# Kernel optimization log

Measured on AMD Instinct MI355X. Metric: run time of the kernel, lower is better.

The kernel has to match this reference:

```python
import jax, jax.numpy as jnp
import numpy as np

BS, EP = 32, 32
N_AGENTS, N_ATOM, EMBED = 8, 51, 32
STATE_DIM, HYP = 128, 64
V_MIN, V_MAX = -10.0, 10.0


def proj(support, probs, v_min, v_max, n_atom):
    # C51 categorical projection of (support, probs) onto the fixed atom grid
    # linspace(v_min, v_max, n_atom). support/probs: [..., M] -> [..., n_atom]
    support, probs = jnp.broadcast_arrays(support, probs)
    delta = (v_max - v_min) / (n_atom - 1)
    b = (jnp.clip(support, v_min, v_max) - v_min) / delta
    l = jnp.floor(b)
    u = jnp.ceil(b)
    eq = (u == l).astype(probs.dtype)  # support exactly on an atom -> all mass to l
    ml = probs * (u - b + eq)
    mu = probs * (b - l)
    shp = probs.shape
    n = int(np.prod(shp[:-1]))
    m = shp[-1]
    rows = jnp.arange(n)[:, None]
    out = jnp.zeros((n, n_atom), probs.dtype)
    out = out.at[rows, l.astype(jnp.int32).reshape(n, m)].add(ml.reshape(n, m))
    out = out.at[rows, u.astype(jnp.int32).reshape(n, m)].add(mu.reshape(n, m))
    return out.reshape(shp[:-1] + (n_atom,))


def bconv(p, q):
    # Full 1D convolution of per-row categorical pmfs (sum of two random vars).
    # p: [N, L], q: [N, M] -> [N, L+M-1], via grouped conv (one group per row).
    N, L = p.shape
    M = q.shape[-1]
    out = jax.lax.conv_general_dilated(
        p[None], jnp.flip(q, -1)[:, None, :],
        window_strides=(1,), padding=[(M - 1, M - 1)],
        feature_group_count=N, dimension_numbers=('NCW', 'OIW', 'NCW'))
    return out[0]


def mlp2(x, w1, b1, w2, b2):
    return jax.nn.relu(x @ w1.T + b1) @ w2.T + b2


def setup_inputs():
    key = jax.random.key(0)
    ks = jax.random.split(key, 20)
    def p(k, shape, s=0.05):
        return jax.random.normal(k, shape, dtype=jnp.float32) * s
    aq = jax.random.uniform(ks[0], (BS, EP, N_AGENTS, N_ATOM), dtype=jnp.float32)
    aq = aq / jnp.sum(aq, -1, keepdims=True)  # valid categorical distributions
    return {
        'agent_qs_distri': aq,
        'states': p(ks[1], (BS, EP, STATE_DIM), 1.0),
        'hw1_w1': p(ks[2], (HYP, STATE_DIM)), 'hw1_b1': p(ks[3], (HYP,)),
        'hw1_w2': p(ks[4], (EMBED * N_AGENTS, HYP)), 'hw1_b2': p(ks[5], (EMBED * N_AGENTS,)),
        'hb1_w': p(ks[6], (EMBED, STATE_DIM)), 'hb1_b': p(ks[7], (EMBED,)),
        'hwf_w1': p(ks[8], (HYP, STATE_DIM)), 'hwf_b1': p(ks[9], (HYP,)),
        'hwf_w2': p(ks[10], (EMBED, HYP)), 'hwf_b2': p(ks[11], (EMBED,)),
        'v_w1': p(ks[12], (EMBED, STATE_DIM)), 'v_b1': p(ks[13], (EMBED,)),
        'v_w2': p(ks[14], (1, EMBED)), 'v_b2': p(ks[15], (1,)),
    }


def reference(agent_qs_distri, states, hw1_w1, hw1_b1, hw1_w2, hw1_b2,
              hb1_w, hb1_b, hwf_w1, hwf_b1, hwf_w2, hwf_b2,
              v_w1, v_b1, v_w2, v_b2):
    bs, ep, n_agents, n_atom = agent_qs_distri.shape
    s = states.reshape(-1, STATE_DIM)
    atoms = jnp.linspace(V_MIN, V_MAX, n_atom).astype(jnp.float32)  # [A]

    w1 = jnp.abs(mlp2(s, hw1_w1, hw1_b1, hw1_w2, hw1_b2)).reshape(bs, ep, EMBED, n_agents)
    b1 = (s @ hb1_w.T + hb1_b).reshape(bs, ep, EMBED)

    # stage 1: scale each agent's support by w1[..., k, i], project back onto atoms
    sup1 = atoms * w1[..., None]                                       # [bs,ep,E,Na,A]
    aw = proj(sup1, agent_qs_distri[:, :, None], V_MIN, V_MAX, n_atom)  # [bs,ep,E,Na,A]
    awf = aw.reshape(-1, n_agents, n_atom)                              # [bs*ep*E,Na,A]
    q = awf[:, 0]
    for i in range(1, n_agents):
        q = bconv(q, awf[:, i])                                         # [.., Na*A-Na+1]
    L1 = n_agents * n_atom - n_agents + 1
    sup = jnp.linspace(n_agents * V_MIN, n_agents * V_MAX, L1).astype(jnp.float32)
    sup = jax.nn.elu(sup + b1[..., None])                               # [bs,ep,E,L1]
    x = proj(sup, q.reshape(bs, ep, EMBED, L1), V_MIN, V_MAX, n_atom)   # [bs,ep,E,A]

    # stage 2: hyper_w_final scaling, convolve across embed dim, add V(s)
    wf = jnp.abs(mlp2(s, hwf_w1, hwf_b1, hwf_w2, hwf_b2)).reshape(bs, ep, EMBED)
    xw = proj(atoms * wf[..., None], x, V_MIN, V_MAX, n_atom)           # [bs,ep,E,A]
    xwf = xw.reshape(-1, EMBED, n_atom)
    q = xwf[:, 0]
    for i in range(1, EMBED):
        q = bconv(q, xwf[:, i])                                         # [bs*ep, E*A-E+1]
    L2 = EMBED * n_atom - EMBED + 1
    v = mlp2(s, v_w1, v_b1, v_w2, v_b2).reshape(bs, ep, 1)
    sup2 = jnp.linspace(EMBED * V_MIN, EMBED * V_MAX, L2).astype(jnp.float32) + v
    return proj(sup2, q.reshape(bs, ep, L2), V_MIN, V_MAX, n_atom)      # [bs,ep,A]
```

## Files before the change

kernel.cpp:

```cpp
#include <hip/hip_runtime.h>
#include <hip/hip_bf16.h>
#include <math.h>

typedef unsigned short u16;

#define WAVE_SYNC() asm volatile("s_waitcnt lgkmcnt(0)" ::: "memory")

__device__ __forceinline__ float bf2f(u16 u) {
  union { unsigned int i; float f; } c;
  c.i = ((unsigned int)u) << 16;
  return c.f;
}
__device__ __forceinline__ float bflo(unsigned int u) {
  union { unsigned int i; float f; } c; c.i = u << 16; return c.f;
}
__device__ __forceinline__ float bfhi(unsigned int u) {
  union { unsigned int i; float f; } c; c.i = u & 0xffff0000u; return c.f;
}
__device__ __forceinline__ u16 f2bf(float f) {
  union { float f; unsigned int i; } c;
  c.f = f;
  unsigned int x = c.i;
  unsigned int r = (x + 0x7fffu + ((x >> 16) & 1u)) >> 16;
  return (u16)r;
}

__device__ __forceinline__ void proj_bounds(float wv, int& ML, int& MH) {
  float smin = (-10.0f + 0.4f * 0.0f)  * wv;
  float smax = (-10.0f + 0.4f * 50.0f) * wv;
  float bmin = (fminf(fmaxf(smin, -10.0f), 10.0f) + 10.0f) / 0.4f;
  float bmax = (fminf(fmaxf(smax, -10.0f), 10.0f) + 10.0f) / 0.4f;
  ML = (int)floorf(bmin);
  MH = (int)ceilf(bmax);
}

template<typename SUPP>
__device__ __forceinline__ void proj_scan(float* __restrict__ g1,
                                          float* __restrict__ g2,
                                          int span, int lane, SUPP supp)
{
  if (lane < 52) g1[lane] = 0.f;
  if (lane < 53) g2[lane] = 0.f;
  float cml = 0.f, cmu = 0.f;
  int ck = -1;
  for (int base = 0; base < span; base += 64) {
    int t = base + lane;
    bool act = (t < span);
    int tc = act ? t : (span - 1);
    float sup, p;
    supp(tc, act, sup, p);
    float c  = fminf(fmaxf(sup, -10.0f), 10.0f);
    float b  = (c + 10.0f) / 0.4f;
    float l  = floorf(b);
    float u  = ceilf(b);
    float eq = (u == l) ? 1.0f : 0.0f;
    float ml = p * (u - b + eq);
    float mu = p * (b - l);
    int   li = (int)l;
    bool last = (base + 64 >= span);
    if (lane == 0 && ck >= 0) {
      if (ck == li) { ml += cml; mu += cmu; }
      else          { g1[ck] = cml; g2[ck + 1] = cmu; }
    }
#pragma unroll
    for (int d = 1; d < 64; d <<= 1) {
      int   lo = __shfl_up(li, d);
      float a1 = __shfl_up(ml, d);
      float a2 = __shfl_up(mu, d);
      bool same = (lane >= d) && (lo == li);
      ml += same ? a1 : 0.f;
      mu += same ? a2 : 0.f;
    }
    int ln = __shfl_down(li, 1);
    bool runend = (lane == 63) ? last : (ln != li);
    if (runend) { g1[li] = ml; g2[li + 1] = mu; }
    if (!last) {
      cml = __shfl(ml, 63);
      cmu = __shfl(mu, 63);
      ck  = __shfl(li, 63);
    }
  }
}

__device__ __forceinline__ void conv_pad2(const float* __restrict__ q,
                                          float* __restrict__ qn,
                                          const float* __restrict__ kvs,
                                          int ML, int W, int T,
                                          int LQ, int HQ, int tid, int nthr)
{
  const int Lout = LQ + ML, Hout = HQ + ML + T;
  for (int J = Lout + tid; J <= Hout; J += nthr) {
    const float* qp = q + (J - ML);
    float acc = 0.f;
    for (int c = 0; c < W; c += 4) {
      float4 k4 = *(const float4*)(kvs + c);
      acc = fmaf(k4.x, qp[-c],     acc);
      acc = fmaf(k4.y, qp[-c - 1], acc);
      acc = fmaf(k4.z, qp[-c - 2], acc);
      acc = fmaf(k4.w, qp[-c - 3], acc);
    }
    qn[J] = acc;
  }
}

__device__ __forceinline__ void conv16(const float* __restrict__ q,
                                       float* __restrict__ qn,
                                       const float* __restrict__ kvs,
                                       int ML, int T,
                                       int LQ, int HQ, int tid, int nthr)
{
  const int Lout = LQ + ML, Hout = HQ + ML + T;
  for (int J = Lout + tid; J <= Hout; J += nthr) {
    const float* qp = q + (J - ML);
    float a0 = 0.f, a1 = 0.f;
#pragma unroll
    for (int c = 0; c < 16; c += 4) {
      float4 k4 = *(const float4*)(kvs + c);
      a0 = fmaf(k4.x, qp[-c],     a0);
      a1 = fmaf(k4.y, qp[-c - 1], a1);
      a0 = fmaf(k4.z, qp[-c - 2], a0);
      a1 = fmaf(k4.w, qp[-c - 3], a1);
    }
    qn[J] = a0 + a1;
  }
}

template<int TA, int TB>
__device__ __forceinline__ float gather_part(const float* __restrict__ pb,
                                             float wv, float j)
{
  float a0 = 0.f, a1 = 0.f, a2 = 0.f, a3 = 0.f;
  const float4* pb4 = (const float4*)pb;
  const float base = 25.0f - j;
#pragma unroll
  for (int t4 = TA; t4 < TB; ++t4) {
    float4 p4 = pb4[t4];
#define G1(PX, TT, AC) { \
    float sup = ((float)(TT) * 0.4f - 10.0f) * wv; \
    float c   = fminf(fmaxf(sup, -10.0f), 10.0f); \
    float d   = fmaf(c, 2.5f, base); \
    AC = fmaf(PX, fmaxf(0.f, 1.0f - fabsf(d)), AC); }
    G1(p4.x, 4 * t4 + 0, a0)
    G1(p4.y, 4 * t4 + 1, a1)
    G1(p4.z, 4 * t4 + 2, a2)
    G1(p4.w, 4 * t4 + 3, a3)
#undef G1
  }
  return (a0 + a1) + (a2 + a3);
}

template<int BF>
__device__ __forceinline__ float ldt(const void* p, int i) {
  if (BF) return bf2f(((const u16*)p)[i]);
  return ((const float*)p)[i];
}

template<int BF>
__device__ __forceinline__ float dot128_t(const void* w, int row, const float* s) {
  float acc = 0.f;
  if (BF) {
    const uint4* p = (const uint4*)((const u16*)w + row * 128);
#pragma unroll
    for (int i = 0; i < 16; ++i) {
      uint4 v = p[i];
      int b = i * 8;
      acc = fmaf(bflo(v.x), s[b + 0], acc); acc = fmaf(bfhi(v.x), s[b + 1], acc);
      acc = fmaf(bflo(v.y), s[b + 2], acc); acc = fmaf(bfhi(v.y), s[b + 3], acc);
      acc = fmaf(bflo(v.z), s[b + 4], acc); acc = fmaf(bfhi(v.z), s[b + 5], acc);
      acc = fmaf(bflo(v.w), s[b + 6], acc); acc = fmaf(bfhi(v.w), s[b + 7], acc);
    }
  } else {
    const float4* p = (const float4*)((const float*)w + row * 128);
#pragma unroll
    for (int i = 0; i < 32; ++i) {
      float4 v = p[i];
      int b = i * 4;
      acc = fmaf(v.x, s[b + 0], acc); acc = fmaf(v.y, s[b + 1], acc);
      acc = fmaf(v.z, s[b + 2], acc); acc = fmaf(v.w, s[b + 3], acc);
    }
  }
  return acc;
}

template<int BF>
__device__ __forceinline__ float dot64_t(const void* w, int row, const float* h) {
  float acc = 0.f;
  if (BF) {
    const uint4* p = (const uint4*)((const u16*)w + row * 64);
#pragma unroll
    for (int i = 0; i < 8; ++i) {
      uint4 v = p[i];
      int b = i * 8;
      acc = fmaf(bflo(v.x), h[b + 0], acc); acc = fmaf(bfhi(v.x), h[b + 1], acc);
      acc = fmaf(bflo(v.y), h[b + 2], acc); acc = fmaf(bfhi(v.y), h[b + 3], acc);
      acc = fmaf(bflo(v.z), h[b + 4], acc); acc = fmaf(bfhi(v.z), h[b + 5], acc);
      acc = fmaf(bflo(v.w), h[b + 6], acc); acc = fmaf(bfhi(v.w), h[b + 7], acc);
    }
  } else {
    const float4* p = (const float4*)((const float*)w + row * 64);
#pragma unroll
    for (int i = 0; i < 16; ++i) {
      float4 v = p[i];
      int b = i * 4;
      acc = fmaf(v.x, h[b + 0], acc); acc = fmaf(v.y, h[b + 1], acc);
      acc = fmaf(v.z, h[b + 2], acc); acc = fmaf(v.w, h[b + 3], acc);
    }
  }
  return acc;
}

template<int BF>
__device__ __forceinline__ void mlp_body(
    const void* states,
    const void* hw1_w1, const void* hw1_b1, const void* hw1_w2, const void* hw1_b2,
    const void* hb1_w,  const void* hb1_b,
    const void* hwf_w1, const void* hwf_b1, const void* hwf_w2, const void* hwf_b2,
    const void* v_w1,   const void* v_b1,   const void* v_w2,   const void* v_b2,
    float* w1_ws, float* b1_ws, float* wf_ws, float* v_ws,
    int n, int tid, float* s, float* h1, float* hf, float* vh)
{
  s[tid]      = ldt<BF>(states, n * 128 + tid);
  s[tid + 64] = ldt<BF>(states, n * 128 + 64 + tid);
  __syncthreads();

  h1[tid] = fmaxf(dot128_t<BF>(hw1_w1, tid, s) + ldt<BF>(hw1_b1, tid), 0.f);
  hf[tid] = fmaxf(dot128_t<BF>(hwf_w1, tid, s) + ldt<BF>(hwf_b1, tid), 0.f);
  if (tid < 32) {
    vh[tid] = fmaxf(dot128_t<BF>(v_w1, tid, s) + ldt<BF>(v_b1, tid), 0.f);
    b1_ws[n * 32 + tid] = dot128_t<BF>(hb1_w, tid, s) + ldt<BF>(hb1_b, tid);
  }
  __syncthreads();

#pragma unroll
  for (int k = 0; k < 4; ++k) {
    int o = tid + 64 * k;
    w1_ws[n * 256 + o] = fabsf(dot64_t<BF>(hw1_w2, o, h1) + ldt<BF>(hw1_b2, o));
  }
  if (tid < 32)
    wf_ws[n * 32 + tid] = fabsf(dot64_t<BF>(hwf_w2, tid, hf) + ldt<BF>(hwf_b2, tid));
  if (tid == 0) {
    float acc = ldt<BF>(v_b2, 0);
    for (int e = 0; e < 32; ++e) acc = fmaf(ldt<BF>(v_w2, e), vh[e], acc);
    v_ws[n] = acc;
  }
}

__global__ __launch_bounds__(64) void k_mlp(
    const void* __restrict__ states,
    const void* __restrict__ hw1_w1, const void* __restrict__ hw1_b1,
    const void* __restrict__ hw1_w2, const void* __restrict__ hw1_b2,
    const void* __restrict__ hb1_w,  const void* __restrict__ hb1_b,
    const void* __restrict__ hwf_w1, const void* __restrict__ hwf_b1,
    const void* __restrict__ hwf_w2, const void* __restrict__ hwf_b2,
    const void* __restrict__ v_w1,   const void* __restrict__ v_b1,
    const void* __restrict__ v_w2,   const void* __restrict__ v_b2,
    float* __restrict__ w1_ws, float* __restrict__ b1_ws,
    float* __restrict__ wf_ws, float* __restrict__ v_ws,
    int* __restrict__ flag)
{
  __shared__ float s[128];
  __shared__ float h1[64];
  __shared__ float hf[64];
  __shared__ float vh[32];
  const int n = blockIdx.x;
  const int tid = threadIdx.x;

  const u16* sr = (const u16*)states;
  unsigned int e0 = (sr[tid] >> 7) & 0xFF;
  unsigned int e1 = (sr[tid + 64] >> 7) & 0xFF;
  unsigned long long bl0 = __ballot(e0 >= 97 && e0 <= 141);
  unsigned long long bl1 = __ballot(e1 >= 97 && e1 <= 141);
  int bf = (__popcll(bl0) + __popcll(bl1) >= 104) ? 1 : 0;
  if (tid == 0) *flag = bf;

  if (bf)
    mlp_body<1>(states, hw1_w1, hw1_b1, hw1_w2, hw1_b2, hb1_w, hb1_b,
                hwf_w1, hwf_b1, hwf_w2, hwf_b2, v_w1, v_b1, v_w2, v_b2,
                w1_ws, b1_ws, wf_ws, v_ws, n, tid, s, h1, hf, vh);
  else
    mlp_body<0>(states, hw1_w1, hw1_b1, hw1_w2, hw1_b2, hb1_w, hb1_b,
                hwf_w1, hwf_b1, hwf_w2, hwf_b2, v_w1, v_b1, v_w2, v_b2,
                w1_ws, b1_ws, wf_ws, v_ws, n, tid, s, h1, hf, vh);
}

__global__ __launch_bounds__(128) void k_perembed(
    const void* __restrict__ aq,
    const float* __restrict__ w1_ws, const float* __restrict__ b1_ws,
    const float* __restrict__ wf_ws, float* __restrict__ xw_ws,
    const int* __restrict__ flag)
{
  __shared__ __align__(16) float Ab[520];
  __shared__ __align__(16) float Bb[520];
  __shared__ __align__(16) float kv_all[8][16];
  __shared__ __align__(16) float kvo[56];
  __shared__ __align__(16) float p_lds[8][52];
  __shared__ float gA[53];
  __shared__ float gB[54];
  __shared__ __align__(16) float pE[2][64];

  const int tid  = threadIdx.x;
  const int wit  = tid >> 6;
  const int lane = tid & 63;
  const int task = blockIdx.x;
  const int n = task >> 5;
  const int e = task & 31;
  const int bf = *flag;

  if (bf) {
    const u16* p = (const u16*)aq + n * 408;
    if (lane < 52) {
#pragma unroll
      for (int k = 0; k < 4; ++k) {
        int a = 4 * wit + k;
        p_lds[a][lane] = (lane < 51) ? bf2f(p[a * 51 + lane]) : 0.f;
      }
    }
  } else {
    const float* p = (const float*)aq + n * 408;
    if (lane < 52) {
#pragma unroll
      for (int k = 0; k < 4; ++k) {
        int a = 4 * wit + k;
        p_lds[a][lane] = (lane < 51) ? p[a * 51 + lane] : 0.f;
      }
    }
  }
  float wreg = (lane < 8) ? w1_ws[n * 256 + e * 8 + lane] : 0.f;
  float b1v  = b1_ws[n * 32 + e];
  float wfv  = wf_ws[n * 32 + e];

  int mlA = 0, mhA = 0;
  if (lane < 8) proj_bounds(wreg, mlA, mhA);
  WAVE_SYNC();

  {
    int a  = 4 * wit + (lane >> 4);
    int jj = lane & 15;
    float wv = __shfl(wreg, a);
    int ML = __shfl(mlA, a);
    int MH = __shfl(mhA, a);
    int T  = MH - ML;
    float K = (25.0f - (float)(ML + jj)) - 25.0f * wv;
    float a0 = 0.f, a1 = 0.f, a2 = 0.f, a3 = 0.f;
    const float4* pb4 = (const float4*)p_lds[a];
#pragma unroll
    for (int t4 = 0; t4 < 13; ++t4) {
      float4 p4 = pb4[t4];
      float d0 = fmaf((float)(4 * t4 + 0), wv, K);
      float d1 = fmaf((float)(4 * t4 + 1), wv, K);
      float d2 = fmaf((float)(4 * t4 + 2), wv, K);
      float d3 = fmaf((float)(4 * t4 + 3), wv, K);
      a0 = fmaf(p4.x, fmaxf(0.f, 1.0f - fabsf(d0)), a0);
      a1 = fmaf(p4.y, fmaxf(0.f, 1.0f - fabsf(d1)), a1);
      a2 = fmaf(p4.z, fmaxf(0.f, 1.0f - fabsf(d2)), a2);
      a3 = fmaf(p4.w, fmaxf(0.f, 1.0f - fabsf(d3)), a3);
    }
    if (T <= 15)
      kv_all[a][jj] = (jj <= T) ? ((a0 + a1) + (a2 + a3)) : 0.f;
  }
  __syncthreads();

  int LQ, HQ;
  float* q = Ab;
  float* qn = Bb;
  {
    float wv0 = __shfl(wreg, 0);
    int ML0 = __shfl(mlA, 0), MH0 = __shfl(mhA, 0);
    int T0 = MH0 - ML0;
    if (tid < 64) {
      if (T0 <= 15) {
        if (lane <= T0) Ab[64 + ML0 + lane] = kv_all[0][lane];
      } else {
        float acc = gather_part<0, 13>(p_lds[0], wv0, (float)(ML0 + lane));
        if (lane <= T0) Ab[64 + ML0 + lane] = acc;
      }
    }
    LQ = 64 + ML0; HQ = 64 + MH0;
  }

  for (int a = 1; a < 8; ++a) {
    float wv = __shfl(wreg, a);
    int ML = __shfl(mlA, a), MH = __shfl(mhA, a);
    int T = MH - ML;
    const float* kvs;
    int W;
    if (T <= 15) {
      kvs = &kv_all[a][0];
      W = 16;
    } else {
      W = (T + 4) & ~3;
      if (tid < 64) {
        float acc = gather_part<0, 13>(p_lds[a], wv, (float)(ML + lane));
        if (lane < W) kvo[lane] = (lane <= T) ? acc : 0.f;
      }
      kvs = kvo;
    }
    if (tid < W - 1) q[LQ - 1 - tid] = 0.f;
    if (tid < T)     q[HQ + 1 + tid] = 0.f;
    __syncthreads();
    if (T <= 15) conv16(q, qn, kvs, ML, T, LQ, HQ, tid, 128);
    else         conv_pad2(q, qn, kvs, ML, W, T, LQ, HQ, tid, 128);
    __syncthreads();
    LQ += ML; HQ += MH;
    float* t_ = q; q = qn; qn = t_;
  }

  if (wit == 0) {
    int span = HQ - LQ + 1;
    int LQl = LQ;
    const float* qf = q;
    proj_scan(gA, gB, span, lane, [&](int t, bool act, float& sup, float& p) {
      int tg = (LQl - 64) + t;
      float raw = (-80.0f + 0.4f * (float)tg) + b1v;
      sup = (raw > 0.f) ? raw : expm1f(raw);
      p = act ? qf[LQl + t] : 0.f;
    });
    WAVE_SYNC();
    float x2v = (lane < 51) ? (gA[lane] + gB[lane]) : 0.f;
    WAVE_SYNC();
    if (lane < 52) p_lds[0][lane] = (lane < 51) ? x2v : 0.f;
  }
  __syncthreads();

  {
    int MLf, MHf;
    proj_bounds(wfv, MLf, MHf);
    float j = (float)(MLf + lane);
    float part = (wit == 0) ? gather_part<0, 7>(p_lds[0], wfv, j)
                            : gather_part<7, 13>(p_lds[0], wfv, j);
    pE[wit][lane] = part;
    __syncthreads();
    if (wit == 0 && lane <= MHf - MLf)
      xw_ws[task * 51 + MLf + lane] = pE[0][lane] + pE[1][lane];
  }
}

__global__ __launch_bounds__(256) void k_final(
    const float* __restrict__ xw_ws, const float* __restrict__ wf_ws,
    const float* __restrict__ v_ws,
    void* __restrict__ out, const int* __restrict__ flag)
{
  __shared__ __align__(16) float bufA[4608];
  __shared__ __align__(16) float bufB[4608];
  __shared__ int meta_s[63];
  __shared__ int meta_l[63];
  __shared__ int meta_ml[32];
  __shared__ int meta_g[6];
  __shared__ int meta_mltot;
  __shared__ float gA[53], gB[54];

  const int n    = blockIdx.x;
  const int tid  = threadIdx.x;
  const int lane = tid & 63;
  const int bf   = *flag;

  float wfreg = (lane < 32) ? wf_ws[n * 32 + lane] : 0.f;
  float vv    = v_ws[n];

  for (int i = tid; i < 4608; i += 256) { bufA[i] = 0.f; bufB[i] = 0.f; }

  if (tid < 64) {
    int ml, mh;
    proj_bounds(wfreg, ml, mh);
    if (lane < 32) meta_ml[lane] = ml;
    int msum = ml;
#pragma unroll
    for (int d = 1; d < 32; d <<= 1) msum += __shfl_xor(msum, d);
    if (lane == 0) meta_mltot = msum;

    int curlen = mh - ml + 1;
    int base = 0, Ncur = 32;
#pragma unroll
    for (int c = 0; c <= 5; ++c) {
      int lm = (lane < Ncur) ? curlen : 0;
#pragma unroll
      for (int d = 1; d < 32; d <<= 1) {
        int o = __shfl_xor(lm, d);
        lm = (o > lm) ? o : lm;
      }
      int G = (lm + 11) & ~3;
      int sp = ((curlen + 3) & ~3) + G;
      int inc = (lane < Ncur) ? sp : 0;
      int v0 = inc;
#pragma unroll
      for (int d = 1; d < 32; d <<= 1) {
        int u = __shfl_up(inc, d);
        if (lane >= d && lane < 32) inc += u;
      }
      if (lane < Ncur) {
        meta_s[base + lane] = 832 + (inc - v0);
        meta_l[base + lane] = curlen;
      }
      if (lane == 0) meta_g[c] = G;
      if (c < 5) {
        int l0 = __shfl(curlen, 2 * lane);
        int l1 = __shfl(curlen, 2 * lane + 1);
        curlen = l0 + l1 - 1;
        base += Ncur;
        Ncur >>= 1;
      }
    }
  }
  __syncthreads();

  {
    int g = tid >> 3, i = tid & 7;
    int s = meta_s[g], l = meta_l[g], ml = meta_ml[g];
    const float* row = xw_ws + (n * 32 + g) * 51 + ml;
    for (int i0 = i; i0 < l; i0 += 8) bufA[s + i0] = row[i0];
  }
  __syncthreads();

#pragma unroll
  for (int c = 1; c <= 5; ++c) {
    const float* bin = (c & 1) ? bufA : bufB;
    float*       bout = (c & 1) ? bufB : bufA;
    const int Nout = 32 >> c;
    const int lg = 3 + c;
    const int gs = 1 << lg;
    const int k  = tid >> lg;
    const int st = tid & (gs - 1);
    const int bc = 64 - (64 >> c);
    const int bp = 64 - (64 >> (c - 1));
    const int i0 = bp + 2 * k;
    const int sA = meta_s[i0];
    const int sB = meta_s[i0 + 1];
    const int lB = meta_l[i0 + 1];
    const int sO = meta_s[bc + k];
    const int lO = meta_l[bc + k];
    const int W  = (lB + 3) & ~3;

    for (int j = st * 2; j < lO; j += gs * 2) {
      const float* Ap = bin + sA + j + 1;
      float a0 = 0.f, a1 = 0.f;
      for (int m = 0; m < W; m += 4) {
        float4 k4 = *(const float4*)(bin + sB + m);
        float v0 = Ap[-m], v1 = Ap[-m - 1], v2 = Ap[-m - 2];
        float v3 = Ap[-m - 3], v4 = Ap[-m - 4];
        a0 = fmaf(k4.x, v1, fmaf(k4.y, v2, fmaf(k4.z, v3, fmaf(k4.w, v4, a0))));
        a1 = fmaf(k4.x, v0, fmaf(k4.y, v1, fmaf(k4.z, v2, fmaf(k4.w, v3, a1))));
      }
      bout[sO + j] = a0;
      if (j + 1 < lO) bout[sO + j + 1] = a1;
    }

    if (c >= 2 && c <= 4) {
      int G = meta_g[c];
      for (int p = tid; p < G; p += 256) bout[832 - G + p] = 0.f;
      for (int k2 = 0; k2 < Nout; ++k2) {
        int ss = meta_s[bc + k2] + meta_l[bc + k2];
        int ee = (k2 + 1 < Nout) ? meta_s[bc + k2 + 1]
                                 : ss + G + 3;
        for (int p = ss + tid; p < ee; p += 256) bout[p] = 0.f;
      }
    }
    __syncthreads();
  }

  if (tid < 64) {
    int s5 = meta_s[62], l5 = meta_l[62], mlt = meta_mltot;
    const float* qf = bufB + s5;
    proj_scan(gA, gB, l5, lane, [&](int t, bool act, float& sup, float& p) {
      int tg = mlt + t;
      sup = (-320.0f + 0.4f * (float)tg) + vv;
      p = act ? qf[t] : 0.f;
    });
    WAVE_SYNC();
    if (lane < 51) {
      float o = gA[lane] + gB[lane];
      if (bf) ((u16*)out)[n * 51 + lane] = f2bf(o);
      else    ((float*)out)[n * 51 + lane] = o;
    }
  }
}

extern "C" void kernel_launch(void* const* d_in, const int* in_sizes, int n_in,
                              void* d_out, int out_size, void* d_ws, size_t ws_size,
                              hipStream_t stream)
{
  float* ws    = (float*)d_ws;
  float* w1_ws = ws;
  float* b1_ws = w1_ws + 1024 * 256;
  float* wf_ws = b1_ws + 1024 * 32;
  float* v_ws  = wf_ws + 1024 * 32;
  float* xw_ws = v_ws  + 1024;
  int*   flag  = (int*)(xw_ws + 1024 * 32 * 51);

  k_mlp<<<1024, 64, 0, stream>>>(d_in[1],
      d_in[2], d_in[3], d_in[4], d_in[5], d_in[6], d_in[7],
      d_in[8], d_in[9], d_in[10], d_in[11], d_in[12], d_in[13],
      d_in[14], d_in[15],
      w1_ws, b1_ws, wf_ws, v_ws, flag);

  k_perembed<<<32768, 128, 0, stream>>>(d_in[0], w1_ws, b1_ws, wf_ws, xw_ws, flag);

  k_final<<<1024, 256, 0, stream>>>(xw_ws, wf_ws, v_ws, d_out, flag);
}
```

Measured before the change: 274.6 us.

## Rework work split across MLP, per-embed and final kernels with LDS atomics

```diff
diff --git a/kernel.cpp b/kernel.cpp
--- a/kernel.cpp
+++ b/kernel.cpp
@@ -32,54 +32,6 @@
   float bmax = (fminf(fmaxf(smax, -10.0f), 10.0f) + 10.0f) / 0.4f;
   ML = (int)floorf(bmin);
   MH = (int)ceilf(bmax);
-}
-
-template<typename SUPP>
-__device__ __forceinline__ void proj_scan(float* __restrict__ g1,
-                                          float* __restrict__ g2,
-                                          int span, int lane, SUPP supp)
-{
-  if (lane < 52) g1[lane] = 0.f;
-  if (lane < 53) g2[lane] = 0.f;
-  float cml = 0.f, cmu = 0.f;
-  int ck = -1;
-  for (int base = 0; base < span; base += 64) {
-    int t = base + lane;
-    bool act = (t < span);
-    int tc = act ? t : (span - 1);
-    float sup, p;
-    supp(tc, act, sup, p);
-    float c  = fminf(fmaxf(sup, -10.0f), 10.0f);
-    float b  = (c + 10.0f) / 0.4f;
-    float l  = floorf(b);
-    float u  = ceilf(b);
-    float eq = (u == l) ? 1.0f : 0.0f;
-    float ml = p * (u - b + eq);
-    float mu = p * (b - l);
-    int   li = (int)l;
-    bool last = (base + 64 >= span);
-    if (lane == 0 && ck >= 0) {
-      if (ck == li) { ml += cml; mu += cmu; }
-      else          { g1[ck] = cml; g2[ck + 1] = cmu; }
-    }
-#pragma unroll
-    for (int d = 1; d < 64; d <<= 1) {
-      int   lo = __shfl_up(li, d);
-      float a1 = __shfl_up(ml, d);
-      float a2 = __shfl_up(mu, d);
-      bool same = (lane >= d) && (lo == li);
-      ml += same ? a1 : 0.f;
-      mu += same ? a2 : 0.f;
-    }
-    int ln = __shfl_down(li, 1);
-    bool runend = (lane == 63) ? last : (ln != li);
-    if (runend) { g1[li] = ml; g2[li + 1] = mu; }
-    if (!last) {
-      cml = __shfl(ml, 63);
-      cmu = __shfl(mu, 63);
-      ck  = __shfl(li, 63);
-    }
-  }
 }
 
 __device__ __forceinline__ void conv_pad2(const float* __restrict__ q,
@@ -115,6 +67,28 @@
     float a0 = 0.f, a1 = 0.f;
 #pragma unroll
     for (int c = 0; c < 16; c += 4) {
+      float4 k4 = *(const float4*)(kvs + c);
+      a0 = fmaf(k4.x, qp[-c],     a0);
+      a1 = fmaf(k4.y, qp[-c - 1], a1);
+      a0 = fmaf(k4.z, qp[-c - 2], a0);
+      a1 = fmaf(k4.w, qp[-c - 3], a1);
+    }
+    qn[J] = a0 + a1;
+  }
+}
+
+__device__ __forceinline__ void conv8(const float* __restrict__ q,
+                                      float* __restrict__ qn,
+                                      const float* __restrict__ kvs,
+                                      int ML, int T,
+                                      int LQ, int HQ, int tid, int nthr)
+{
+  const int Lout = LQ + ML, Hout = HQ + ML + T;
+  for (int J = Lout + tid; J <= Hout; J += nthr) {
+    const float* qp = q + (J - ML);
+    float a0 = 0.f, a1 = 0.f;
+#pragma unroll
+    for (int c = 0; c < 8; c += 4) {
       float4 k4 = *(const float4*)(kvs + c);
       a0 = fmaf(k4.x, qp[-c],     a0);
       a1 = fmaf(k4.y, qp[-c - 1], a1);
@@ -210,42 +184,41 @@
 }
 
 template<int BF>
-__device__ __forceinline__ void mlp_body(
+__device__ __forceinline__ void mlp_par(
     const void* states,
     const void* hw1_w1, const void* hw1_b1, const void* hw1_w2, const void* hw1_b2,
     const void* hb1_w,  const void* hb1_b,
     const void* hwf_w1, const void* hwf_b1, const void* hwf_w2, const void* hwf_b2,
     const void* v_w1,   const void* v_b1,   const void* v_w2,   const void* v_b2,
     float* w1_ws, float* b1_ws, float* wf_ws, float* v_ws,
-    int n, int tid, float* s, float* h1, float* hf, float* vh)
-{
-  s[tid]      = ldt<BF>(states, n * 128 + tid);
-  s[tid + 64] = ldt<BF>(states, n * 128 + 64 + tid);
+    float* s_st, float* h1, float* hf, float* vh, int n, int tid)
+{
+  if (tid < 128) s_st[tid] = ldt<BF>(states, n * 128 + tid);
   __syncthreads();
-
-  h1[tid] = fmaxf(dot128_t<BF>(hw1_w1, tid, s) + ldt<BF>(hw1_b1, tid), 0.f);
-  hf[tid] = fmaxf(dot128_t<BF>(hwf_w1, tid, s) + ldt<BF>(hwf_b1, tid), 0.f);
-  if (tid < 32) {
-    vh[tid] = fmaxf(dot128_t<BF>(v_w1, tid, s) + ldt<BF>(v_b1, tid), 0.f);
-    b1_ws[n * 32 + tid] = dot128_t<BF>(hb1_w, tid, s) + ldt<BF>(hb1_b, tid);
-  }
+  if (tid < 64)
+    h1[tid] = fmaxf(dot128_t<BF>(hw1_w1, tid, s_st) + ldt<BF>(hw1_b1, tid), 0.f);
+  else if (tid < 128)
+    hf[tid - 64] = fmaxf(dot128_t<BF>(hwf_w1, tid - 64, s_st) + ldt<BF>(hwf_b1, tid - 64), 0.f);
+  else if (tid < 160)
+    vh[tid - 128] = fmaxf(dot128_t<BF>(v_w1, tid - 128, s_st) + ldt<BF>(v_b1, tid - 128), 0.f);
+  else if (tid < 192)
+    b1_ws[n * 32 + tid - 160] = dot128_t<BF>(hb1_w, tid - 160, s_st) + ldt<BF>(hb1_b, tid - 160);
   __syncthreads();
-
-#pragma unroll
-  for (int k = 0; k < 4; ++k) {
-    int o = tid + 64 * k;
-    w1_ws[n * 256 + o] = fabsf(dot64_t<BF>(hw1_w2, o, h1) + ldt<BF>(hw1_b2, o));
-  }
-  if (tid < 32)
-    wf_ws[n * 32 + tid] = fabsf(dot64_t<BF>(hwf_w2, tid, hf) + ldt<BF>(hwf_b2, tid));
-  if (tid == 0) {
-    float acc = ldt<BF>(v_b2, 0);
-    for (int e = 0; e < 32; ++e) acc = fmaf(ldt<BF>(v_w2, e), vh[e], acc);
-    v_ws[n] = acc;
-  }
-}
-
-__global__ __launch_bounds__(64) void k_mlp(
+  if (tid < 256)
+    w1_ws[n * 256 + tid] = fabsf(dot64_t<BF>(hw1_w2, tid, h1) + ldt<BF>(hw1_b2, tid));
+  else if (tid < 288)
+    wf_ws[n * 32 + tid - 256] = fabsf(dot64_t<BF>(hwf_w2, tid - 256, hf) + ldt<BF>(hwf_b2, tid - 256));
+  else {
+    int l2 = tid - 288;
+    float part = vh[l2] * ldt<BF>(v_w2, l2);
+    part += __shfl_xor(part, 1);  part += __shfl_xor(part, 2);
+    part += __shfl_xor(part, 4);  part += __shfl_xor(part, 8);
+    part += __shfl_xor(part, 16);
+    if (l2 == 0) v_ws[n] = part + ldt<BF>(v_b2, 0);
+  }
+}
+
+__global__ __launch_bounds__(320) void k_mlp(
     const void* __restrict__ states,
     const void* __restrict__ hw1_w1, const void* __restrict__ hw1_b1,
     const void* __restrict__ hw1_w2, const void* __restrict__ hw1_b2,
@@ -258,29 +231,32 @@
     float* __restrict__ wf_ws, float* __restrict__ v_ws,
     int* __restrict__ flag)
 {
-  __shared__ float s[128];
-  __shared__ float h1[64];
-  __shared__ float hf[64];
-  __shared__ float vh[32];
+  __shared__ float s_st[128];
+  __shared__ float h1[64], hf[64], vh[32];
+  __shared__ int sh_flag;
   const int n = blockIdx.x;
   const int tid = threadIdx.x;
 
-  const u16* sr = (const u16*)states;
-  unsigned int e0 = (sr[tid] >> 7) & 0xFF;
-  unsigned int e1 = (sr[tid + 64] >> 7) & 0xFF;
-  unsigned long long bl0 = __ballot(e0 >= 97 && e0 <= 141);
-  unsigned long long bl1 = __ballot(e1 >= 97 && e1 <= 141);
-  int bf = (__popcll(bl0) + __popcll(bl1) >= 104) ? 1 : 0;
-  if (tid == 0) *flag = bf;
+  if (tid < 64) {
+    const u16* sr = (const u16*)states;
+    unsigned int e0 = (sr[tid] >> 7) & 0xFF;
+    unsigned int e1 = (sr[tid + 64] >> 7) & 0xFF;
+    unsigned long long bl0 = __ballot(e0 >= 97 && e0 <= 141);
+    unsigned long long bl1 = __ballot(e1 >= 97 && e1 <= 141);
+    int bfv = (__popcll(bl0) + __popcll(bl1) >= 104) ? 1 : 0;
+    if (tid == 0) { sh_flag = bfv; *flag = bfv; }
+  }
+  __syncthreads();
+  const int bf = sh_flag;
 
   if (bf)
-    mlp_body<1>(states, hw1_w1, hw1_b1, hw1_w2, hw1_b2, hb1_w, hb1_b,
-                hwf_w1, hwf_b1, hwf_w2, hwf_b2, v_w1, v_b1, v_w2, v_b2,
-                w1_ws, b1_ws, wf_ws, v_ws, n, tid, s, h1, hf, vh);
+    mlp_par<1>(states, hw1_w1, hw1_b1, hw1_w2, hw1_b2, hb1_w, hb1_b,
+               hwf_w1, hwf_b1, hwf_w2, hwf_b2, v_w1, v_b1, v_w2, v_b2,
+               w1_ws, b1_ws, wf_ws, v_ws, s_st, h1, hf, vh, n, tid);
   else
-    mlp_body<0>(states, hw1_w1, hw1_b1, hw1_w2, hw1_b2, hb1_w, hb1_b,
-                hwf_w1, hwf_b1, hwf_w2, hwf_b2, v_w1, v_b1, v_w2, v_b2,
-                w1_ws, b1_ws, wf_ws, v_ws, n, tid, s, h1, hf, vh);
+    mlp_par<0>(states, hw1_w1, hw1_b1, hw1_w2, hw1_b2, hb1_w, hb1_b,
+               hwf_w1, hwf_b1, hwf_w2, hwf_b2, v_w1, v_b1, v_w2, v_b2,
+               w1_ws, b1_ws, wf_ws, v_ws, s_st, h1, hf, vh, n, tid);
 }
 
 __global__ __launch_bounds__(128) void k_perembed(
@@ -289,19 +265,13 @@
     const float* __restrict__ wf_ws, float* __restrict__ xw_ws,
     const int* __restrict__ flag)
 {
-  __shared__ __align__(16) float Ab[520];
-  __shared__ __align__(16) float Bb[520];
-  __shared__ __align__(16) float kv_all[8][16];
-  __shared__ __align__(16) float kvo[56];
-  __shared__ __align__(16) float p_lds[8][52];
-  __shared__ float gA[53];
-  __shared__ float gB[54];
-  __shared__ __align__(16) float pE[2][64];
+  __shared__ __align__(16) float P[8 * 52];
+  __shared__ __align__(16) float TS[2][1332];
 
   const int tid  = threadIdx.x;
-  const int wit  = tid >> 6;
+  const int w    = tid >> 6;
   const int lane = tid & 63;
-  const int task = blockIdx.x;
+  const int task = blockIdx.x * 2 + w;
   const int n = task >> 5;
   const int e = task & 31;
   const int bf = *flag;
@@ -311,8 +281,8 @@
     if (lane < 52) {
 #pragma unroll
       for (int k = 0; k < 4; ++k) {
-        int a = 4 * wit + k;
-        p_lds[a][lane] = (lane < 51) ? bf2f(p[a * 51 + lane]) : 0.f;
+        int a = 4 * w + k;
+        P[a * 52 + lane] = (lane < 51) ? bf2f(p[a * 51 + lane]) : 0.f;
       }
     }
   } else {
@@ -320,8 +290,8 @@
     if (lane < 52) {
 #pragma unroll
       for (int k = 0; k < 4; ++k) {
-        int a = 4 * wit + k;
-        p_lds[a][lane] = (lane < 51) ? p[a * 51 + lane] : 0.f;
+        int a = 4 * w + k;
+        P[a * 52 + lane] = (lane < 51) ? p[a * 51 + lane] : 0.f;
       }
     }
   }
@@ -331,10 +301,18 @@
 
   int mlA = 0, mhA = 0;
   if (lane < 8) proj_bounds(wreg, mlA, mhA);
-  WAVE_SYNC();
-
-  {
-    int a  = 4 * wit + (lane >> 4);
+  __syncthreads();
+
+  float* Ab  = TS[w];
+  float* Bb  = Ab + 520;
+  float* kv  = Ab + 1040;
+  float* kvo = Ab + 1168;
+  float* x2  = Ab + 1224;
+  float* g   = Ab + 1276;
+
+#pragma unroll
+  for (int r = 0; r < 2; ++r) {
+    int a  = 4 * r + (lane >> 4);
     int jj = lane & 15;
     float wv = __shfl(wreg, a);
     int ML = __shfl(mlA, a);
@@ -342,7 +320,7 @@
     int T  = MH - ML;
     float K = (25.0f - (float)(ML + jj)) - 25.0f * wv;
     float a0 = 0.f, a1 = 0.f, a2 = 0.f, a3 = 0.f;
-    const float4* pb4 = (const float4*)p_lds[a];
+    const float4* pb4 = (const float4*)(P + a * 52);
 #pragma unroll
     for (int t4 = 0; t4 < 13; ++t4) {
       float4 p4 = pb4[t4];
@@ -356,9 +334,9 @@
       a3 = fmaf(p4.w, fmaxf(0.f, 1.0f - fabsf(d3)), a3);
     }
     if (T <= 15)
-      kv_all[a][jj] = (jj <= T) ? ((a0 + a1) + (a2 + a3)) : 0.f;
-  }
-  __syncthreads();
+      kv[a * 16 + jj] = (jj <= T) ? ((a0 + a1) + (a2 + a3)) : 0.f;
+  }
+  WAVE_SYNC();
 
   int LQ, HQ;
   float* q = Ab;
@@ -367,14 +345,13 @@
     float wv0 = __shfl(wreg, 0);
     int ML0 = __shfl(mlA, 0), MH0 = __shfl(mhA, 0);
     int T0 = MH0 - ML0;
-    if (tid < 64) {
-      if (T0 <= 15) {
-        if (lane <= T0) Ab[64 + ML0 + lane] = kv_all[0][lane];
-      } else {
-        float acc = gather_part<0, 13>(p_lds[0], wv0, (float)(ML0 + lane));
-        if (lane <= T0) Ab[64 + ML0 + lane] = acc;
-      }
-    }
+    if (T0 <= 15) {
+      if (lane <= T0) Ab[64 + ML0 + lane] = kv[lane];
+    } else {
+      float acc = gather_part<0, 13>(P, wv0, (float)(ML0 + lane));
+      if (lane <= T0) Ab[64 + ML0 + lane] = acc;
+    }
+    WAVE_SYNC();
     LQ = 64 + ML0; HQ = 64 + MH0;
   }
 
@@ -385,57 +362,78 @@
     const float* kvs;
     int W;
     if (T <= 15) {
-      kvs = &kv_all[a][0];
-      W = 16;
+      kvs = kv + a * 16;
+      W = (T <= 7) ? 8 : 16;
     } else {
+      float acc = gather_part<0, 13>(P + a * 52, wv, (float)(ML + lane));
       W = (T + 4) & ~3;
-      if (tid < 64) {
-        float acc = gather_part<0, 13>(p_lds[a], wv, (float)(ML + lane));
-        if (lane < W) kvo[lane] = (lane <= T) ? acc : 0.f;
-      }
+      if (lane < W) kvo[lane] = (lane <= T) ? acc : 0.f;
       kvs = kvo;
     }
-    if (tid < W - 1) q[LQ - 1 - tid] = 0.f;
-    if (tid < T)     q[HQ + 1 + tid] = 0.f;
-    __syncthreads();
-    if (T <= 15) conv16(q, qn, kvs, ML, T, LQ, HQ, tid, 128);
-    else         conv_pad2(q, qn, kvs, ML, W, T, LQ, HQ, tid, 128);
-    __syncthreads();
+    if (lane < W - 1) q[LQ - 1 - lane] = 0.f;
+    if (lane < T)     q[HQ + 1 + lane] = 0.f;
+    WAVE_SYNC();
+    if (T <= 7)       conv8 (q, qn, kvs, ML, T, LQ, HQ, lane, 64);
+    else if (T <= 15) conv16(q, qn, kvs, ML, T, LQ, HQ, lane, 64);
+    else              conv_pad2(q, qn, kvs, ML, W, T, LQ, HQ, lane, 64);
+    WAVE_SYNC();
     LQ += ML; HQ += MH;
     float* t_ = q; q = qn; qn = t_;
   }
 
-  if (wit == 0) {
+  {
+    if (lane < 53) g[lane] = 0.f;
+    WAVE_SYNC();
     int span = HQ - LQ + 1;
-    int LQl = LQ;
-    const float* qf = q;
-    proj_scan(gA, gB, span, lane, [&](int t, bool act, float& sup, float& p) {
-      int tg = (LQl - 64) + t;
-      float raw = (-80.0f + 0.4f * (float)tg) + b1v;
-      sup = (raw > 0.f) ? raw : expm1f(raw);
-      p = act ? qf[LQl + t] : 0.f;
-    });
+    for (int base = 0; base < span; base += 64) {
+      int t = base + lane;
+      if (t < span) {
+        int tg = (LQ - 64) + t;
+        float raw = (-80.0f + 0.4f * (float)tg) + b1v;
+        float sup = (raw > 0.f) ? raw : expm1f(raw);
+        float c  = fminf(fmaxf(sup, -10.0f), 10.0f);
+        float b  = (c + 10.0f) / 0.4f;
+        float l  = floorf(b);
+        float u  = ceilf(b);
+        float eq = (u == l) ? 1.0f : 0.0f;
+        float p  = q[LQ + t];
+        int   li = (int)l;
+        atomicAdd(&g[li],     p * (u - b + eq));
+        atomicAdd(&g[li + 1], p * (b - l));
+      }
+    }
     WAVE_SYNC();
-    float x2v = (lane < 51) ? (gA[lane] + gB[lane]) : 0.f;
-    WAVE_SYNC();
-    if (lane < 52) p_lds[0][lane] = (lane < 51) ? x2v : 0.f;
-  }
-  __syncthreads();
+  }
+  if (lane < 52) x2[lane] = (lane < 51) ? g[lane] : 0.f;
+  WAVE_SYNC();
 
   {
     int MLf, MHf;
     proj_bounds(wfv, MLf, MHf);
-    float j = (float)(MLf + lane);
-    float part = (wit == 0) ? gather_part<0, 7>(p_lds[0], wfv, j)
-                            : gather_part<7, 13>(p_lds[0], wfv, j);
-    pE[wit][lane] = part;
-    __syncthreads();
-    if (wit == 0 && lane <= MHf - MLf)
-      xw_ws[task * 51 + MLf + lane] = pE[0][lane] + pE[1][lane];
-  }
-}
-
-__global__ __launch_bounds__(256) void k_final(
+    int Tf = MHf - MLf;
+    if (Tf <= 15) {
+      int q4 = lane >> 4, jj = lane & 15;
+      float K = (25.0f - (float)(MLf + jj)) - 25.0f * wfv;
+      float acc = 0.f;
+#pragma unroll
+      for (int k = 0; k < 13; ++k) {
+        int t = q4 + 4 * k;
+        float d = fmaf((float)t, wfv, K);
+        acc = fmaf(x2[t], fmaxf(0.f, 1.0f - fabsf(d)), acc);
+      }
+      acc += __shfl_xor(acc, 16);
+      acc += __shfl_xor(acc, 32);
+      if (lane <= Tf)
+        xw_ws[task * 51 + MLf + lane] = acc;
+    } else {
+      float acc = gather_part<0, 13>(x2, wfv, (float)(MLf + lane));
+      if (lane <= Tf)
+        xw_ws[task * 51 + MLf + lane] = acc;
+    }
+  }
+}
+
+__global__ __launch_bounds__(512) void k_final(
     const float* __restrict__ xw_ws, const float* __restrict__ wf_ws,
     const float* __restrict__ v_ws,
     void* __restrict__ out, const int* __restrict__ flag)
@@ -447,19 +445,20 @@
   __shared__ int meta_ml[32];
   __shared__ int meta_g[6];
   __shared__ int meta_mltot;
-  __shared__ float gA[53], gB[54];
+  __shared__ float gA[53];
 
   const int n    = blockIdx.x;
   const int tid  = threadIdx.x;
   const int lane = tid & 63;
   const int bf   = *flag;
 
-  float wfreg = (lane < 32) ? wf_ws[n * 32 + lane] : 0.f;
-  float vv    = v_ws[n];
-
-  for (int i = tid; i < 4608; i += 256) { bufA[i] = 0.f; bufB[i] = 0.f; }
+  float vv = v_ws[n];
+
+  for (int i = tid; i < 4608; i += 512) { bufA[i] = 0.f; bufB[i] = 0.f; }
+  if (tid < 53) gA[tid] = 0.f;
 
   if (tid < 64) {
+    float wfreg = (lane < 32) ? wf_ws[n * 32 + lane] : 0.f;
     int ml, mh;
     proj_bounds(wfreg, ml, mh);
     if (lane < 32) meta_ml[lane] = ml;
@@ -504,10 +503,10 @@
   __syncthreads();
 
   {
-    int g = tid >> 3, i = tid & 7;
-    int s = meta_s[g], l = meta_l[g], ml = meta_ml[g];
+    int g = tid >> 4, i3 = tid & 15;
+    int s2 = meta_s[g], l2 = meta_l[g], ml = meta_ml[g];
     const float* row = xw_ws + (n * 32 + g) * 51 + ml;
-    for (int i0 = i; i0 < l; i0 += 8) bufA[s + i0] = row[i0];
+    for (int i0 = i3; i0 < l2; i0 += 16) bufA[s2 + i0] = row[i0];
   }
   __syncthreads();
 
@@ -516,7 +515,7 @@
     const float* bin = (c & 1) ? bufA : bufB;
     float*       bout = (c & 1) ? bufB : bufA;
     const int Nout = 32 >> c;
-    const int lg = 3 + c;
+    const int lg = 4 + c;
     const int gs = 1 << lg;
     const int k  = tid >> lg;
     const int st = tid & (gs - 1);
@@ -546,31 +545,39 @@
 
     if (c >= 2 && c <= 4) {
       int G = meta_g[c];
-      for (int p = tid; p < G; p += 256) bout[832 - G + p] = 0.f;
+      for (int p = tid; p < G; p += 512) bout[832 - G + p] = 0.f;
       for (int k2 = 0; k2 < Nout; ++k2) {
         int ss = meta_s[bc + k2] + meta_l[bc + k2];
         int ee = (k2 + 1 < Nout) ? meta_s[bc + k2 + 1]
                                  : ss + G + 3;
-        for (int p = ss + tid; p < ee; p += 256) bout[p] = 0.f;
+        for (int p = ss + tid; p < ee; p += 512) bout[p] = 0.f;
       }
     }
     __syncthreads();
   }
 
-  if (tid < 64) {
+  {
     int s5 = meta_s[62], l5 = meta_l[62], mlt = meta_mltot;
     const float* qf = bufB + s5;
-    proj_scan(gA, gB, l5, lane, [&](int t, bool act, float& sup, float& p) {
+    for (int t = tid; t < l5; t += 512) {
       int tg = mlt + t;
-      sup = (-320.0f + 0.4f * (float)tg) + vv;
-      p = act ? qf[t] : 0.f;
-    });
-    WAVE_SYNC();
-    if (lane < 51) {
-      float o = gA[lane] + gB[lane];
-      if (bf) ((u16*)out)[n * 51 + lane] = f2bf(o);
-      else    ((float*)out)[n * 51 + lane] = o;
-    }
+      float sup = (-320.0f + 0.4f * (float)tg) + vv;
+      float c  = fminf(fmaxf(sup, -10.0f), 10.0f);
+      float b  = (c + 10.0f) / 0.4f;
+      float l  = floorf(b);
+      float u  = ceilf(b);
+      float eq = (u == l) ? 1.0f : 0.0f;
+      float p  = qf[t];
+      int   li = (int)l;
+      atomicAdd(&gA[li],     p * (u - b + eq));
+      atomicAdd(&gA[li + 1], p * (b - l));
+    }
+  }
+  __syncthreads();
+  if (tid < 51) {
+    float o = gA[tid];
+    if (bf) ((u16*)out)[n * 51 + tid] = f2bf(o);
+    else    ((float*)out)[n * 51 + tid] = o;
   }
 }
 
@@ -586,13 +593,13 @@
   float* xw_ws = v_ws  + 1024;
   int*   flag  = (int*)(xw_ws + 1024 * 32 * 51);
 
-  k_mlp<<<1024, 64, 0, stream>>>(d_in[1],
+  k_mlp<<<1024, 320, 0, stream>>>(d_in[1],
       d_in[2], d_in[3], d_in[4], d_in[5], d_in[6], d_in[7],
       d_in[8], d_in[9], d_in[10], d_in[11], d_in[12], d_in[13],
       d_in[14], d_in[15],
       w1_ws, b1_ws, wf_ws, v_ws, flag);
 
-  k_perembed<<<32768, 128, 0, stream>>>(d_in[0], w1_ws, b1_ws, wf_ws, xw_ws, flag);
-
-  k_final<<<1024, 256, 0, stream>>>(xw_ws, wf_ws, v_ws, d_out, flag);
-}
+  k_perembed<<<16384, 128, 0, stream>>>(d_in[0], w1_ws, b1_ws, wf_ws, xw_ws, flag);
+
+  k_final<<<1024, 512, 0, stream>>>(xw_ws, wf_ws, v_ws, d_out, flag);
+}
```

New measurement: 254.8 us. 1.08x faster.
